# Performance work log

Hardware: AMD Instinct MI355X
Metric: run time of the kernel (lower is better)

## Reference

```python
import jax, jax.numpy as jnp
from jax import lax
import numpy as np

HID = 32

def setup_inputs() -> dict:
    key = jax.random.key(0)
    ks = jax.random.split(key, 8)
    B, T = 4096, 1024
    x = jax.random.normal(ks[0], (B, T, 1), dtype=jnp.float32)
    h = jnp.zeros((1, B, HID), dtype=jnp.float32)
    s = 1.0 / np.sqrt(HID)  # PyTorch GRU init scale
    W_ih = jax.random.uniform(ks[1], (3 * HID, 1), minval=-s, maxval=s, dtype=jnp.float32)
    W_hh = jax.random.uniform(ks[2], (3 * HID, HID), minval=-s, maxval=s, dtype=jnp.float32)
    b_ih = jax.random.uniform(ks[3], (3 * HID,), minval=-s, maxval=s, dtype=jnp.float32)
    b_hh = jax.random.uniform(ks[4], (3 * HID,), minval=-s, maxval=s, dtype=jnp.float32)
    W_out = jax.random.uniform(ks[5], (1, HID), minval=-s, maxval=s, dtype=jnp.float32)
    b_out = jax.random.uniform(ks[6], (1,), minval=-s, maxval=s, dtype=jnp.float32)
    return {"x": x, "h": h, "W_ih": W_ih, "W_hh": W_hh, "b_ih": b_ih,
            "b_hh": b_hh, "W_out": W_out, "b_out": b_out}

def _gru(x, h0, W_ih, W_hh, b_ih, b_hh):
    # Precompute input projections for all timesteps: [B, T, 3H]
    xi = jnp.einsum('bti,gi->btg', x, W_ih) + b_ih

    def step(h, xi_t):
        gh = h @ W_hh.T + b_hh                      # [B, 3H]
        ir, iz, inn = jnp.split(xi_t, 3, axis=-1)
        hr, hz, hn = jnp.split(gh, 3, axis=-1)
        r = jax.nn.sigmoid(ir + hr)
        z = jax.nn.sigmoid(iz + hz)
        n = jnp.tanh(inn + r * hn)
        h_new = (1.0 - z) * n + z * h               # PyTorch GRU update
        return h_new, h_new

    h_last, hs = lax.scan(step, h0, jnp.swapaxes(xi, 0, 1))  # time-major scan
    return jnp.swapaxes(hs, 0, 1), h_last            # [B,T,H], [B,H]

def reference(x, h, W_ih, W_hh, b_ih, b_hh, W_out, b_out):
    h0 = h[0]                                        # [B, H]
    seq, h_last = _gru(x, h0, W_ih, W_hh, b_ih, b_hh)
    out = jnp.einsum('bth,oh->bto', seq, W_out) + b_out  # [B, T, 1]
    return out, h_last[None]                         # h: [1, B, H]
```

## Files before the change

kernel.cpp:

```cpp
#include <hip/hip_runtime.h>
#include <hip/hip_bf16.h>

#define BATCH 4096
#define T_LEN 1024
#define HID 32
#define CT 64
#define NCHUNK (T_LEN / CT)
#define L2E 1.4426950408889634f

typedef short bf16x8 __attribute__((ext_vector_type(8)));
typedef short short4v __attribute__((ext_vector_type(4)));
typedef float f32x4 __attribute__((ext_vector_type(4)));

__device__ __forceinline__ short bf16hi_rne(float f, float* back) {
    unsigned u = __float_as_uint(f);
    unsigned r = (u + 0x7fffu + ((u >> 16) & 1u)) & 0xffff0000u;
    *back = __uint_as_float(r);
    return (short)(r >> 16);
}
__device__ __forceinline__ float fast_rcp(float x)  { return __builtin_amdgcn_rcpf(x); }
__device__ __forceinline__ float fast_exp2(float x) { return __builtin_amdgcn_exp2f(x); }

#define MFMA __builtin_amdgcn_mfma_f32_16x16x32_bf16

__global__ void __launch_bounds__(256, 1)
gru_fused6(const float* __restrict__ xg, const float* __restrict__ h0g,
           const float* __restrict__ Wih, const float* __restrict__ Whh,
           const float* __restrict__ bih, const float* __restrict__ bhh,
           const float* __restrict__ Wout, const float* __restrict__ boutp,
           float* __restrict__ outp)
{
    const int tid  = threadIdx.x;
    const int v    = tid >> 6;
    const int half = v & 1;
    const int sub  = v >> 1;
    const int l    = tid & 63;
    const int rg   = (l >> 4) & 3;
    const int cl   = l & 15;
    const int b0   = blockIdx.x << 4;

    __shared__ float xbuf[16][68];
    __shared__ float po[16][16][68];
    __shared__ __align__(16) short ex[2][2][4][16][8];
    const int PAR = 2 * 4 * 16 * 8;

    bf16x8 A1[3][2], A2[3][2];
    const int phicl = 4 * (cl >> 2) + 2 * sub + (cl & 1);
#pragma unroll
    for (int q = 0; q < 3; ++q) {
        const int m = 2 * q + half;
        const float sc = (q < 2) ? L2E : 2.0f * L2E;
        const int grow = m * 16 + phicl;
#pragma unroll
        for (int kh = 0; kh < 2; ++kh)
#pragma unroll
            for (int qs = 0; qs < 4; ++qs) {
                float wv = Whh[grow * HID + 16 * kh + 4 * rg + qs] * sc;
                float hf, d;
                short hi = bf16hi_rne(wv, &hf);
                short lo = bf16hi_rne(wv - hf, &d);
                int shi = (qs < 2) ? qs : qs + 2;
                int slo = (qs < 2) ? qs + 2 : qs + 4;
                A1[q][kh][shi] = hi;  A1[q][kh][slo] = hi;
                A2[q][kh][shi] = lo;  A2[q][kh][slo] = 0;
            }
    }
    float wr4[4], br4[4], wz4[4], bz4[4], wn2[2], bn2[2], wo2[2];
    f32x4 bN;
#pragma unroll
    for (int u = 0; u < 4; ++u) {
        int rrow = 4 * rg + 2 * sub + (u & 1);
        int gr = half * 16 + rrow;
        int gz = (2 + half) * 16 + rrow;
        int gn = (4 + half) * 16 + rrow;
        wr4[u] = L2E * Wih[gr];  br4[u] = L2E * (bih[gr] + bhh[gr]);
        wz4[u] = L2E * Wih[gz];  bz4[u] = L2E * (bih[gz] + bhh[gz]);
        bN[u]  = 2.0f * L2E * bhh[gn];
    }
#pragma unroll
    for (int u = 0; u < 2; ++u) {
        int rrow = 4 * rg + 2 * sub + u;
        int gn = (4 + half) * 16 + rrow;
        wn2[u] = 2.0f * L2E * Wih[gn];
        bn2[u] = 2.0f * L2E * bih[gn];
        wo2[u] = Wout[half * 16 + rrow];
    }
    const float bout = boutp[0];

    float h2[2];
#pragma unroll
    for (int u = 0; u < 2; ++u)
        h2[u] = h0g[(size_t)(b0 + cl) * HID + 16 * half + 4 * rg + 2 * sub + u];
    bf16x8 B0, B1;
#pragma unroll
    for (int qs = 0; qs < 4; ++qs) {
        int shi = (qs < 2) ? qs : qs + 2;
        int slo = (qs < 2) ? qs + 2 : qs + 4;
        float hv0 = h0g[(size_t)(b0 + cl) * HID + 4 * rg + qs];
        float hf;
        B0[shi] = bf16hi_rne(hv0, &hf);
        B0[slo] = (short)(__float_as_uint(hv0 - hf) >> 16);
        float hv1 = h0g[(size_t)(b0 + cl) * HID + 16 + 4 * rg + qs];
        B1[shi] = bf16hi_rne(hv1, &hf);
        B1[slo] = (short)(__float_as_uint(hv1 - hf) >> 16);
    }

    short* const exW        = &ex[0][half][rg][cl][sub * 4];
    const short* const exR0 = &ex[0][0][rg][cl][0];
    const short* const exR1 = &ex[0][1][rg][cl][0];

    for (int tc = 0; tc < NCHUNK; ++tc) {
        if (tc > 0) {
            int row = tid >> 4, seg = tid & 15;
            f32x4 sacc = {bout, bout, bout, bout};
#pragma unroll
            for (int g = 0; g < 16; ++g)
                sacc += *reinterpret_cast<const f32x4*>(&po[g][row][seg * 4]);
            *reinterpret_cast<f32x4*>(
                &outp[(size_t)(b0 + row) * T_LEN + (tc - 1) * CT + seg * 4]) = sacc;
        }
        {
            int row = tid >> 4, seg = tid & 15;
            *reinterpret_cast<f32x4*>(&xbuf[row][seg * 4]) =
                *reinterpret_cast<const f32x4*>(
                    &xg[(size_t)(b0 + row) * T_LEN + tc * CT + seg * 4]);
        }
        __syncthreads();
        f32x4 xq = *reinterpret_cast<const f32x4*>(&xbuf[cl][0]);

        for (int qt = 0; qt < 16; ++qt) {
            f32x4 xqn = *reinterpret_cast<const f32x4*>(&xbuf[cl][((qt + 1) & 15) * 4]);
            f32x4 opv;
#pragma unroll
            for (int s = 0; s < 4; ++s) {
                const float xv = xq[s];
                f32x4 iR, iZ;
#pragma unroll
                for (int u = 0; u < 4; ++u) {
                    iR[u] = fmaf(xv, wr4[u], br4[u]);
                    iZ[u] = fmaf(xv, wz4[u], bz4[u]);
                }
                f32x4 aR, aZ, aN;
                aR = MFMA(A1[0][0], B0, iR, 0, 0, 0);
                aZ = MFMA(A1[1][0], B0, iZ, 0, 0, 0);
                aN = MFMA(A1[2][0], B0, bN, 0, 0, 0);
                aR = MFMA(A2[0][0], B0, aR, 0, 0, 0);
                aZ = MFMA(A2[1][0], B0, aZ, 0, 0, 0);
                aN = MFMA(A2[2][0], B0, aN, 0, 0, 0);
                aR = MFMA(A1[0][1], B1, aR, 0, 0, 0);
                aZ = MFMA(A1[1][1], B1, aZ, 0, 0, 0);
                aN = MFMA(A1[2][1], B1, aN, 0, 0, 0);
                aR = MFMA(A2[0][1], B1, aR, 0, 0, 0);
                aZ = MFMA(A2[1][1], B1, aZ, 0, 0, 0);
                aN = MFMA(A2[2][1], B1, aN, 0, 0, 0);

                float op = 0.f;
                short4v pkv;
#pragma unroll
                for (int u = 0; u < 2; ++u) {
                    float rr = fast_rcp(1.f + fast_exp2(-aR[u]));
                    float zz = fast_rcp(1.f + fast_exp2(-aZ[u]));
                    float np = fmaf(rr, aN[u], fmaf(xv, wn2[u], bn2[u]));
                    float nn = fmaf(-2.f, fast_rcp(1.f + fast_exp2(np)), 1.f);
                    float hv = fmaf(zz, h2[u] - nn, nn);
                    h2[u] = hv;
                    op = fmaf(hv, wo2[u], op);
                    float hf;
                    pkv[u]     = bf16hi_rne(hv, &hf);
                    pkv[2 + u] = (short)(__float_as_uint(hv - hf) >> 16);
                }
                opv[s] = op;
                *reinterpret_cast<short4v*>(exW + (s & 1) * PAR) = pkv;
                if (s == 3)
                    *reinterpret_cast<f32x4*>(&po[v * 4 + rg][cl][qt * 4]) = opv;
                __syncthreads();
                B0 = *reinterpret_cast<const bf16x8*>(exR0 + (s & 1) * PAR);
                B1 = *reinterpret_cast<const bf16x8*>(exR1 + (s & 1) * PAR);
            }
            xq = xqn;
        }
    }

    {
        int row = tid >> 4, seg = tid & 15;
        f32x4 sacc = {bout, bout, bout, bout};
#pragma unroll
        for (int g = 0; g < 16; ++g)
            sacc += *reinterpret_cast<const f32x4*>(&po[g][row][seg * 4]);
        *reinterpret_cast<f32x4*>(
            &outp[(size_t)(b0 + row) * T_LEN + (NCHUNK - 1) * CT + seg * 4]) = sacc;
    }

#pragma unroll
    for (int u = 0; u < 2; ++u)
        outp[(size_t)BATCH * T_LEN + (size_t)(b0 + cl) * HID
             + 16 * half + 4 * rg + 2 * sub + u] = h2[u];
}

extern "C" void kernel_launch(void* const* d_in, const int* in_sizes, int n_in,
                              void* d_out, int out_size, void* d_ws, size_t ws_size,
                              hipStream_t stream) {
    const float* x     = (const float*)d_in[0];
    const float* h0    = (const float*)d_in[1];
    const float* Wih   = (const float*)d_in[2];
    const float* Whh   = (const float*)d_in[3];
    const float* bihv  = (const float*)d_in[4];
    const float* bhhv  = (const float*)d_in[5];
    const float* Woutv = (const float*)d_in[6];
    const float* boutv = (const float*)d_in[7];
    float* out = (float*)d_out;

    gru_fused6<<<dim3(BATCH / 16), dim3(256), 0, stream>>>(
        x, h0, Wih, Whh, bihv, bhhv, Woutv, boutv, out);
}
```

Measured before the change: 400.3 us.

## Restructure split-bf16 recurrent matmul to three-product form with planar hidden exchange

The recurrent W_hh·h product is regrouped from two K-halves with interleaved hi/lo packing (12 MFMAs per step) into a single K=32 layout using separate hi and lo bf16 planes. It computes hi·hi + hi·lo + lo·hi (9 MFMAs per step) and drops the lo·lo term. The shared-memory exchange of the hidden state changes to match: separate hi and lo planes with padded rows, written as 32-bit words and read back as two bf16x8 vectors. This shortens the MFMA dependency chain on the serial per-timestep critical path, at the cost of slightly lower precision and a different LDS access pattern.

```diff
diff --git a/kernel.cpp b/kernel.cpp
--- a/kernel.cpp
+++ b/kernel.cpp
@@ -9,7 +9,6 @@
 #define L2E 1.4426950408889634f
 
 typedef short bf16x8 __attribute__((ext_vector_type(8)));
-typedef short short4v __attribute__((ext_vector_type(4)));
 typedef float f32x4 __attribute__((ext_vector_type(4)));
 
 __device__ __forceinline__ short bf16hi_rne(float f, float* back) {
@@ -24,7 +23,7 @@
 #define MFMA __builtin_amdgcn_mfma_f32_16x16x32_bf16
 
 __global__ void __launch_bounds__(256, 1)
-gru_fused6(const float* __restrict__ xg, const float* __restrict__ h0g,
+gru_fused7(const float* __restrict__ xg, const float* __restrict__ h0g,
            const float* __restrict__ Wih, const float* __restrict__ Whh,
            const float* __restrict__ bih, const float* __restrict__ bhh,
            const float* __restrict__ Wout, const float* __restrict__ boutp,
@@ -41,29 +40,22 @@
 
     __shared__ float xbuf[16][68];
     __shared__ float po[16][16][68];
-    __shared__ __align__(16) short ex[2][2][4][16][8];
-    const int PAR = 2 * 4 * 16 * 8;
-
-    bf16x8 A1[3][2], A2[3][2];
+    __shared__ __align__(16) short ex[2][2][16][40];
+    const int PAR = 2 * 16 * 40;
+
+    bf16x8 Ahi[3], Alo[3];
     const int phicl = 4 * (cl >> 2) + 2 * sub + (cl & 1);
 #pragma unroll
     for (int q = 0; q < 3; ++q) {
         const int m = 2 * q + half;
         const float sc = (q < 2) ? L2E : 2.0f * L2E;
-        const int grow = m * 16 + phicl;
-#pragma unroll
-        for (int kh = 0; kh < 2; ++kh)
-#pragma unroll
-            for (int qs = 0; qs < 4; ++qs) {
-                float wv = Whh[grow * HID + 16 * kh + 4 * rg + qs] * sc;
-                float hf, d;
-                short hi = bf16hi_rne(wv, &hf);
-                short lo = bf16hi_rne(wv - hf, &d);
-                int shi = (qs < 2) ? qs : qs + 2;
-                int slo = (qs < 2) ? qs + 2 : qs + 4;
-                A1[q][kh][shi] = hi;  A1[q][kh][slo] = hi;
-                A2[q][kh][shi] = lo;  A2[q][kh][slo] = 0;
-            }
+#pragma unroll
+        for (int s = 0; s < 8; ++s) {
+            float wv = Whh[(m * 16 + phicl) * HID + 8 * rg + s] * sc;
+            float hf;
+            Ahi[q][s] = bf16hi_rne(wv, &hf);
+            Alo[q][s] = (short)(__float_as_uint(wv - hf) >> 16);
+        }
     }
     float wr4[4], br4[4], wz4[4], bz4[4], wn2[2], bn2[2], wo2[2];
     f32x4 bN;
@@ -91,23 +83,21 @@
 #pragma unroll
     for (int u = 0; u < 2; ++u)
         h2[u] = h0g[(size_t)(b0 + cl) * HID + 16 * half + 4 * rg + 2 * sub + u];
-    bf16x8 B0, B1;
-#pragma unroll
-    for (int qs = 0; qs < 4; ++qs) {
-        int shi = (qs < 2) ? qs : qs + 2;
-        int slo = (qs < 2) ? qs + 2 : qs + 4;
-        float hv0 = h0g[(size_t)(b0 + cl) * HID + 4 * rg + qs];
+    bf16x8 Bhi, Blo;
+#pragma unroll
+    for (int s = 0; s < 8; ++s) {
+        float hv = h0g[(size_t)(b0 + cl) * HID + 8 * rg + s];
         float hf;
-        B0[shi] = bf16hi_rne(hv0, &hf);
-        B0[slo] = (short)(__float_as_uint(hv0 - hf) >> 16);
-        float hv1 = h0g[(size_t)(b0 + cl) * HID + 16 + 4 * rg + qs];
-        B1[shi] = bf16hi_rne(hv1, &hf);
-        B1[slo] = (short)(__float_as_uint(hv1 - hf) >> 16);
-    }
-
-    short* const exW        = &ex[0][half][rg][cl][sub * 4];
-    const short* const exR0 = &ex[0][0][rg][cl][0];
-    const short* const exR1 = &ex[0][1][rg][cl][0];
+        Bhi[s] = bf16hi_rne(hv, &hf);
+        Blo[s] = (short)(__float_as_uint(hv - hf) >> 16);
+    }
+
+    short* const exFlat = &ex[0][0][0][0];
+    const int j0 = 16 * half + 4 * rg + 2 * sub;
+    short* const exWh = exFlat + cl * 40 + j0;
+    short* const exWl = exFlat + (16 + cl) * 40 + j0;
+    const short* const exRh = exFlat + cl * 40 + 8 * rg;
+    const short* const exRl = exFlat + (16 + cl) * 40 + 8 * rg;
 
     for (int tc = 0; tc < NCHUNK; ++tc) {
         if (tc > 0) {
@@ -141,21 +131,18 @@
                     iZ[u] = fmaf(xv, wz4[u], bz4[u]);
                 }
                 f32x4 aR, aZ, aN;
-                aR = MFMA(A1[0][0], B0, iR, 0, 0, 0);
-                aZ = MFMA(A1[1][0], B0, iZ, 0, 0, 0);
-                aN = MFMA(A1[2][0], B0, bN, 0, 0, 0);
-                aR = MFMA(A2[0][0], B0, aR, 0, 0, 0);
-                aZ = MFMA(A2[1][0], B0, aZ, 0, 0, 0);
-                aN = MFMA(A2[2][0], B0, aN, 0, 0, 0);
-                aR = MFMA(A1[0][1], B1, aR, 0, 0, 0);
-                aZ = MFMA(A1[1][1], B1, aZ, 0, 0, 0);
-                aN = MFMA(A1[2][1], B1, aN, 0, 0, 0);
-                aR = MFMA(A2[0][1], B1, aR, 0, 0, 0);
-                aZ = MFMA(A2[1][1], B1, aZ, 0, 0, 0);
-                aN = MFMA(A2[2][1], B1, aN, 0, 0, 0);
+                aR = MFMA(Ahi[0], Bhi, iR, 0, 0, 0);
+                aZ = MFMA(Ahi[1], Bhi, iZ, 0, 0, 0);
+                aN = MFMA(Ahi[2], Bhi, bN, 0, 0, 0);
+                aR = MFMA(Ahi[0], Blo, aR, 0, 0, 0);
+                aZ = MFMA(Ahi[1], Blo, aZ, 0, 0, 0);
+                aN = MFMA(Ahi[2], Blo, aN, 0, 0, 0);
+                aR = MFMA(Alo[0], Bhi, aR, 0, 0, 0);
+                aZ = MFMA(Alo[1], Bhi, aZ, 0, 0, 0);
+                aN = MFMA(Alo[2], Bhi, aN, 0, 0, 0);
 
                 float op = 0.f;
-                short4v pkv;
+                unsigned hw = 0, lw = 0;
 #pragma unroll
                 for (int u = 0; u < 2; ++u) {
                     float rr = fast_rcp(1.f + fast_exp2(-aR[u]));
@@ -166,16 +153,19 @@
                     h2[u] = hv;
                     op = fmaf(hv, wo2[u], op);
                     float hf;
-                    pkv[u]     = bf16hi_rne(hv, &hf);
-                    pkv[2 + u] = (short)(__float_as_uint(hv - hf) >> 16);
+                    unsigned hu = (unsigned)(unsigned short)bf16hi_rne(hv, &hf);
+                    unsigned lu = (__float_as_uint(hv - hf) >> 16);
+                    hw |= hu << (16 * u);
+                    lw |= lu << (16 * u);
                 }
                 opv[s] = op;
-                *reinterpret_cast<short4v*>(exW + (s & 1) * PAR) = pkv;
+                *reinterpret_cast<unsigned*>(exWh + (s & 1) * PAR) = hw;
+                *reinterpret_cast<unsigned*>(exWl + (s & 1) * PAR) = lw;
                 if (s == 3)
                     *reinterpret_cast<f32x4*>(&po[v * 4 + rg][cl][qt * 4]) = opv;
                 __syncthreads();
-                B0 = *reinterpret_cast<const bf16x8*>(exR0 + (s & 1) * PAR);
-                B1 = *reinterpret_cast<const bf16x8*>(exR1 + (s & 1) * PAR);
+                Bhi = *reinterpret_cast<const bf16x8*>(exRh + (s & 1) * PAR);
+                Blo = *reinterpret_cast<const bf16x8*>(exRl + (s & 1) * PAR);
             }
             xq = xqn;
         }
@@ -210,6 +200,6 @@
     const float* boutv = (const float*)d_in[7];
     float* out = (float*)d_out;
 
-    gru_fused6<<<dim3(BATCH / 16), dim3(256), 0, stream>>>(
+    gru_fused7<<<dim3(BATCH / 16), dim3(256), 0, stream>>>(
         x, h0, Wih, Whh, bihv, bhhv, Woutv, boutv, out);
 }
```

Result: faster. 389.5 us (-2.7%).
